# Optimization experiments

Measured on AMD Instinct MI355X. Metric: run time of the kernel, lower is better.

## Reference

```python
import jax, jax.numpy as jnp
import numpy as np

N_TREE = 200
DEPTH = 3
N_LEAF = 2 ** (DEPTH + 1) - 1      # 15 internal decision nodes
N_LEAVES = N_LEAF + 1              # 16 leaves
N_NODE = 64
BATCH = 2048
D_FEAT = 512
LR = 0.01


def _leaf_paths(depth):
    """For each of the 2^(depth+1) leaves, the internal-node index and the
    left/right bit at every level (matches the tf.gather index construction:
    bit==0 -> take p, bit==1 -> take 1-p; children of node n are 2n+1, 2n+2)."""
    L = 2 ** (depth + 1)
    nodes = np.zeros((L, depth + 1), np.int32)
    bits = np.zeros((L, depth + 1), np.int32)
    for l in range(L):
        node = 0
        for d in range(depth + 1):
            bit = (l >> (depth - d)) & 1
            nodes[l, d] = node
            bits[l, d] = bit
            node = 2 * node + 1 + bit
    return nodes, bits

_NODES, _BITS = _leaf_paths(DEPTH)


def setup_inputs() -> dict:
    key = jax.random.key(0)
    ks = jax.random.split(key, 9)
    u = lambda k, s: jax.random.uniform(k, s, jnp.float32, -0.05, 0.05)  # keras 'uniform' init
    return {
        "x": jax.random.normal(ks[0], (BATCH, D_FEAT), jnp.float32),
        "y_true": jax.random.normal(ks[1], (BATCH, 1), jnp.float32),
        "w_t": u(ks[2], (N_TREE, D_FEAT, N_NODE)),
        "b_t": u(ks[3], (N_TREE, N_NODE)),
        "w_d": u(ks[4], (N_TREE, N_NODE, N_LEAF)),
        "b_d": u(ks[5], (N_TREE, N_LEAF)),
        "w_l": u(ks[6], (N_TREE, N_LEAVES)),
        "b_l": u(ks[7], (N_TREE,)),
        "f_0": jnp.full((1,), 0.5, jnp.float32),
    }


def reference(x, y_true, w_t, b_t, w_d, b_d, w_l, b_l, f_0):
    B = x.shape[0]
    # Batched per-tree small MLP (the 200-iteration Python loop in the original).
    # Dropout is identity at inference.
    h = jax.nn.relu(jnp.einsum('bd,tdn->tbn', x, w_t) + b_t[:, None, :])        # [T,B,N_NODE]
    p = jax.nn.sigmoid(jnp.einsum('tbn,tnl->tbl', h, w_d) + b_d[:, None, :])    # [T,B,15]
    # Soft binary-tree routing: mu[t,b,leaf] = prod over path of p or (1-p).
    # This reproduces the tiled-index tf.gather construction exactly.
    pn = p[..., _NODES]                                                         # [T,B,16,DEPTH+1]
    q = jnp.where(_BITS == 1, 1.0 - pn, pn)
    mu = jnp.prod(q, axis=-1)                                                   # [T,B,16]
    # Per-tree leaf score with tanh.
    f = jnp.tanh(jnp.einsum('tbl,tl->tb', mu, w_l) + b_l[:, None])              # [T,B]
    # Sequential boosting accumulation: predict_k = f_0 + lr * sum_{i<k} f_i.
    cum = f_0 + LR * jnp.cumsum(f.T, axis=1)                                    # [B,T]
    py_x = jnp.concatenate([jnp.broadcast_to(f_0[None, :], (B, 1)), cum], axis=1)  # [B,T+1]
    return py_x
```

## Files before the change

kernel.cpp:

```cpp
#include <hip/hip_runtime.h>

#define T_TREES 200
#define BATCH   2048
#define D_FEAT  512
#define N_NODE  64
#define LR      0.01f

typedef __attribute__((__ext_vector_type__(8)))  __bf16 bf16x8;
typedef __attribute__((__ext_vector_type__(16))) float  f32x16;

__device__ __forceinline__ unsigned short f32_to_bf16(float f) {
    unsigned u = __float_as_uint(f);
    u += 0x7FFFu + ((u >> 16) & 1u);
    return (unsigned short)(u >> 16);
}

__device__ __forceinline__ void gload_lds16(const void* g, void* l) {
    __builtin_amdgcn_global_load_lds(
        (__attribute__((address_space(1))) void*)(void*)g,
        (__attribute__((address_space(3))) void*)l,
        16, 0, 0);
}


__global__ __launch_bounds__(256) void prep_x(const float* __restrict__ x,
                                              unsigned short* __restrict__ x_p) {
    __shared__ float tile[64 * 65];
    int mb = blockIdx.x >> 3;
    int slab = blockIdx.x & 7;
    const float* src = x + (mb * 64) * D_FEAT + slab * 64;
    #pragma unroll
    for (int p = 0; p < 16; ++p) {
        int idx = p * 256 + threadIdx.x;
        int r = idx >> 6, c = idx & 63;
        tile[r * 65 + c] = src[r * D_FEAT + c];
    }
    __syncthreads();
    int mt = mb >> 1, mq = mb & 1;
    unsigned short* dst = x_p + mt * 65536 + slab * 8192 + mq * 512;
    #pragma unroll
    for (int p = 0; p < 8; ++p) {
        int idx = p * 256 + threadIdx.x;
        int kgl = idx >> 8;
        int r   = (idx >> 2) & 63;
        int jp  = idx & 3;
        ushort2 o;
        o.x = f32_to_bf16(tile[r * 65 + kgl * 8 + jp * 2]);
        o.y = f32_to_bf16(tile[r * 65 + kgl * 8 + jp * 2 + 1]);
        *(ushort2*)(dst + kgl * 1024 + r * 8 + jp * 2) = o;
    }
}

__global__ __launch_bounds__(256) void prep_wt(const float* __restrict__ w_t,
                                               unsigned short* __restrict__ w_p) {
    __shared__ float tile[64 * 65];
    int t = blockIdx.x >> 3, slab = blockIdx.x & 7;
    const float* src = w_t + t * (D_FEAT * N_NODE) + slab * 64 * N_NODE;
    #pragma unroll
    for (int p = 0; p < 16; ++p) {
        int idx = p * 256 + threadIdx.x;
        int d = idx >> 6, n = idx & 63;
        tile[d * 65 + n] = src[d * N_NODE + n];
    }
    __syncthreads();
    unsigned short* dst = w_p + (t >> 1) * 65536 + slab * 8192 + (t & 1) * 512;
    #pragma unroll
    for (int p = 0; p < 8; ++p) {
        int idx = p * 256 + threadIdx.x;
        int kgl = idx >> 8;
        int n   = (idx >> 2) & 63;
        int jp  = idx & 3;
        ushort2 o;
        o.x = f32_to_bf16(tile[(kgl * 8 + jp * 2) * 65 + n]);
        o.y = f32_to_bf16(tile[(kgl * 8 + jp * 2 + 1) * 65 + n]);
        *(ushort2*)(dst + kgl * 1024 + n * 8 + jp * 2) = o;
    }
}

__global__ void prep_wd(const float* __restrict__ w_d, unsigned short* __restrict__ w_dt) {
    int i = blockIdx.x * 256 + threadIdx.x;
    int n = i & 63;
    int l = (i >> 6) & 31;
    int t = i >> 11;
    float v = (l < 15) ? w_d[(t * 64 + n) * 15 + l] : 0.f;
    w_dt[i] = f32_to_bf16(v);
}

__global__ __launch_bounds__(256, 3) void gbdt_main(
    const unsigned short* __restrict__ x_p,
    const unsigned short* __restrict__ w_p,
    const unsigned short* __restrict__ w_dt,
    const float* __restrict__ b_t,
    const float* __restrict__ b_d,
    const float* __restrict__ w_l,
    const float* __restrict__ b_l,
    float* __restrict__ f_ws)
{
    __shared__ alignas(16) char smem[36864];
    unsigned short* Hs = (unsigned short*)smem;
    float*          Pf = (float*)smem;

    const int tid    = threadIdx.x;
    const int lane   = tid & 63;
    const int w      = tid >> 6;
    const int lane31 = lane & 31;
    const int kh     = lane >> 5;
    const int wm     = w >> 1;
    const int wn     = w & 1;

    const int xcd  = blockIdx.x & 7;
    const int slot = blockIdx.x >> 3;
    const int mt   = slot & 15;
    const int pj   = slot >> 4;
    const int pair = xcd * 13 + pj;
    if (pair >= 100) return;
    const int t0 = pair * 2;
    const int m0 = mt * 128;

    const char* ga = (const char*)(x_p + mt * 65536) + tid * 16;
    const char* gb = (const char*)(w_p + pair * 65536) + tid * 16;

    f32x16 acc[2][2];
    #pragma unroll
    for (int mb = 0; mb < 2; ++mb)
        #pragma unroll
        for (int nb = 0; nb < 2; ++nb)
            acc[mb][nb] = (f32x16)(0.f);

    #pragma unroll
    for (int i = 0; i < 2; ++i) {
        gload_lds16(ga + i * 4096, smem + tid * 16 + i * 4096);
        gload_lds16(gb + i * 4096, smem + 8192 + tid * 16 + i * 4096);
    }

    const int aoff = (wm * 64 + lane31) * 16;
    const int boff = 8192 + (wn * 64 + lane31) * 16;

    for (int c = 0; c < 16; ++c) {
        __syncthreads();
        if (c < 15) {
            char* nx = smem + ((c + 1) & 1) * 16384;
            #pragma unroll
            for (int i = 0; i < 2; ++i) {
                gload_lds16(ga + (c + 1) * 8192 + i * 4096, nx + tid * 16 + i * 4096);
                gload_lds16(gb + (c + 1) * 8192 + i * 4096, nx + 8192 + tid * 16 + i * 4096);
            }
        }
        const char* buf = smem + (c & 1) * 16384;
        #pragma unroll
        for (int s2 = 0; s2 < 2; ++s2) {
            const int kgl = 2 * s2 + kh;
            bf16x8 av[2], bv[2];
            #pragma unroll
            for (int mb = 0; mb < 2; ++mb)
                av[mb] = *(const bf16x8*)(buf + aoff + kgl * 2048 + mb * 512);
            #pragma unroll
            for (int nb = 0; nb < 2; ++nb)
                bv[nb] = *(const bf16x8*)(buf + boff + kgl * 2048 + nb * 512);
            #pragma unroll
            for (int mb = 0; mb < 2; ++mb)
                #pragma unroll
                for (int nb = 0; nb < 2; ++nb)
                    acc[mb][nb] = __builtin_amdgcn_mfma_f32_32x32x16_bf16(
                        av[mb], bv[nb], acc[mb][nb], 0, 0, 0);
        }
    }

    __syncthreads();

    #pragma unroll
    for (int nb = 0; nb < 2; ++nb) {
        float btv = b_t[(t0 + wn) * 64 + nb * 32 + lane31];
        #pragma unroll
        for (int mb = 0; mb < 2; ++mb)
            #pragma unroll
            for (int r = 0; r < 16; ++r) {
                int m = wm * 64 + mb * 32 + (r & 3) + 8 * (r >> 2) + 4 * kh;
                float h = fmaxf(acc[mb][nb][r] + btv, 0.f);
                Hs[wn * 8704 + m * 68 + nb * 32 + lane31] = f32_to_bf16(h);
            }
    }
    __syncthreads();

    f32x16 acc2[2] = { (f32x16)(0.f), (f32x16)(0.f) };
    const unsigned short* pW = w_dt + (t0 + wn) * 2048 + lane31 * 64 + kh * 8;
    #pragma unroll
    for (int s = 0; s < 4; ++s) {
        bf16x8 bv = *(const bf16x8*)(pW + s * 16);
        #pragma unroll
        for (int i = 0; i < 2; ++i) {
            const unsigned short* pH =
                Hs + wn * 8704 + (wm * 64 + i * 32 + lane31) * 68 + s * 16 + kh * 8;
            bf16x8 av = *(const bf16x8*)pH;
            acc2[i] = __builtin_amdgcn_mfma_f32_32x32x16_bf16(av, bv, acc2[i], 0, 0, 0);
        }
    }
    __syncthreads();

    if (lane31 < 15) {
        float bdv = b_d[(t0 + wn) * 15 + lane31];
        #pragma unroll
        for (int i = 0; i < 2; ++i)
            #pragma unroll
            for (int r = 0; r < 16; ++r) {
                int m = wm * 64 + i * 32 + (r & 3) + 8 * (r >> 2) + 4 * kh;
                float lg = acc2[i][r] + bdv;
                Pf[(wn * 128 + m) * 17 + lane31] = 1.f / (1.f + __expf(-lg));
            }
    }
    __syncthreads();

    {
        int m = tid & 127;
        int j = tid >> 7;
        int t = t0 + j;
        float pv[15];
        #pragma unroll
        for (int i = 0; i < 15; ++i) pv[i] = Pf[(j * 128 + m) * 17 + i];
        float facc = 0.f;
        #pragma unroll
        for (int leaf = 0; leaf < 16; ++leaf) {
            float mu = 1.f;
            int node = 0;
            #pragma unroll
            for (int d = 0; d < 4; ++d) {
                int bit = (leaf >> (3 - d)) & 1;
                float p = pv[node];
                mu *= bit ? (1.f - p) : p;
                node = 2 * node + 1 + bit;
            }
            facc += mu * w_l[t * 16 + leaf];
        }
        f_ws[(m0 + m) * T_TREES + t] = tanhf(facc + b_l[t]);
    }
}

__global__ void scan_k(const float* __restrict__ f_ws, const float* __restrict__ f0p,
                       float* __restrict__ out) {
    int b = blockIdx.x, tid = threadIdx.x;
    int lane = tid & 63, wid = tid >> 6;
    float f0 = f0p[0];
    float x = (tid < T_TREES) ? f_ws[b * T_TREES + tid] : 0.f;
    #pragma unroll
    for (int off = 1; off < 64; off <<= 1) {
        float y = __shfl_up(x, off, 64);
        if (lane >= off) x += y;
    }
    __shared__ float wsum[4];
    if (lane == 63) wsum[wid] = x;
    __syncthreads();
    float base = 0.f;
    for (int i = 0; i < wid; ++i) base += wsum[i];
    float incl = x + base;
    if (tid == 0) out[b * (T_TREES + 1)] = f0;
    if (tid < T_TREES) out[b * (T_TREES + 1) + 1 + tid] = f0 + LR * incl;
}

extern "C" void kernel_launch(void* const* d_in, const int* in_sizes, int n_in,
                              void* d_out, int out_size, void* d_ws, size_t ws_size,
                              hipStream_t stream) {
    const float* x   = (const float*)d_in[0];
    const float* w_t = (const float*)d_in[2];
    const float* b_t = (const float*)d_in[3];
    const float* w_d = (const float*)d_in[4];
    const float* b_d = (const float*)d_in[5];
    const float* w_l = (const float*)d_in[6];
    const float* b_l = (const float*)d_in[7];
    const float* f_0 = (const float*)d_in[8];
    float* out = (float*)d_out;

    char* ws = (char*)d_ws;
    unsigned short* x_p  = (unsigned short*)(ws);
    unsigned short* w_p  = (unsigned short*)(ws + 2097152);
    unsigned short* w_dt = (unsigned short*)(ws + 15204352);
    float*          f_ws = (float*)(ws + 16023552);

    prep_x  <<< 256, 256, 0, stream>>>(x, x_p);
    prep_wt <<<1600, 256, 0, stream>>>(w_t, w_p);
    prep_wd <<<1600, 256, 0, stream>>>(w_d, w_dt);
    gbdt_main<<<1664, 256, 0, stream>>>(x_p, w_p, w_dt, b_t, b_d, w_l, b_l, f_ws);
    scan_k<<<BATCH, 256, 0, stream>>>(f_ws, f_0, out);
}
```

Baseline: 134.1 us.

## Merge prep kernels and load A operand directly into registers

Fuses the three preprocessing kernels into a single launch with block-range dispatch, removing two kernel launches. In the main GEMM, the x tile is now read straight from global memory into registers and double-buffered there, while only the weight tile goes through LDS. This halves the LDS staging buffer, which lowers shared memory use and lets the launch bound ask for 4 blocks per CU instead of 3. The trade-off is more register pressure and direct global loads of A that are not coalesced through LDS.

```diff
diff --git a/kernel.cpp b/kernel.cpp
--- a/kernel.cpp
+++ b/kernel.cpp
@@ -22,71 +22,70 @@
         16, 0, 0);
 }
 
-
-__global__ __launch_bounds__(256) void prep_x(const float* __restrict__ x,
-                                              unsigned short* __restrict__ x_p) {
+__global__ __launch_bounds__(256) void prep_all(
+    const float* __restrict__ x, const float* __restrict__ w_t,
+    const float* __restrict__ w_d,
+    unsigned short* __restrict__ x_p, unsigned short* __restrict__ w_p,
+    unsigned short* __restrict__ w_dt) {
     __shared__ float tile[64 * 65];
-    int mb = blockIdx.x >> 3;
-    int slab = blockIdx.x & 7;
-    const float* src = x + (mb * 64) * D_FEAT + slab * 64;
-    #pragma unroll
-    for (int p = 0; p < 16; ++p) {
-        int idx = p * 256 + threadIdx.x;
-        int r = idx >> 6, c = idx & 63;
-        tile[r * 65 + c] = src[r * D_FEAT + c];
-    }
-    __syncthreads();
-    int mt = mb >> 1, mq = mb & 1;
-    unsigned short* dst = x_p + mt * 65536 + slab * 8192 + mq * 512;
-    #pragma unroll
-    for (int p = 0; p < 8; ++p) {
-        int idx = p * 256 + threadIdx.x;
-        int kgl = idx >> 8;
-        int r   = (idx >> 2) & 63;
-        int jp  = idx & 3;
-        ushort2 o;
-        o.x = f32_to_bf16(tile[r * 65 + kgl * 8 + jp * 2]);
-        o.y = f32_to_bf16(tile[r * 65 + kgl * 8 + jp * 2 + 1]);
-        *(ushort2*)(dst + kgl * 1024 + r * 8 + jp * 2) = o;
-    }
-}
-
-__global__ __launch_bounds__(256) void prep_wt(const float* __restrict__ w_t,
-                                               unsigned short* __restrict__ w_p) {
-    __shared__ float tile[64 * 65];
-    int t = blockIdx.x >> 3, slab = blockIdx.x & 7;
-    const float* src = w_t + t * (D_FEAT * N_NODE) + slab * 64 * N_NODE;
-    #pragma unroll
-    for (int p = 0; p < 16; ++p) {
-        int idx = p * 256 + threadIdx.x;
-        int d = idx >> 6, n = idx & 63;
-        tile[d * 65 + n] = src[d * N_NODE + n];
-    }
-    __syncthreads();
-    unsigned short* dst = w_p + (t >> 1) * 65536 + slab * 8192 + (t & 1) * 512;
-    #pragma unroll
-    for (int p = 0; p < 8; ++p) {
-        int idx = p * 256 + threadIdx.x;
-        int kgl = idx >> 8;
-        int n   = (idx >> 2) & 63;
-        int jp  = idx & 3;
-        ushort2 o;
-        o.x = f32_to_bf16(tile[(kgl * 8 + jp * 2) * 65 + n]);
-        o.y = f32_to_bf16(tile[(kgl * 8 + jp * 2 + 1) * 65 + n]);
-        *(ushort2*)(dst + kgl * 1024 + n * 8 + jp * 2) = o;
-    }
-}
-
-__global__ void prep_wd(const float* __restrict__ w_d, unsigned short* __restrict__ w_dt) {
-    int i = blockIdx.x * 256 + threadIdx.x;
-    int n = i & 63;
-    int l = (i >> 6) & 31;
-    int t = i >> 11;
-    float v = (l < 15) ? w_d[(t * 64 + n) * 15 + l] : 0.f;
-    w_dt[i] = f32_to_bf16(v);
-}
-
-__global__ __launch_bounds__(256, 3) void gbdt_main(
+    int b = blockIdx.x;
+    if (b < 256) {
+        int mb = b >> 3, slab = b & 7;
+        const float* src = x + (mb * 64) * D_FEAT + slab * 64;
+        #pragma unroll
+        for (int p = 0; p < 16; ++p) {
+            int idx = p * 256 + threadIdx.x;
+            int r = idx >> 6, c = idx & 63;
+            tile[r * 65 + c] = src[r * D_FEAT + c];
+        }
+        __syncthreads();
+        int mt = mb >> 1, mq = mb & 1;
+        unsigned short* dst = x_p + mt * 65536 + slab * 8192 + mq * 512;
+        #pragma unroll
+        for (int p = 0; p < 8; ++p) {
+            int idx = p * 256 + threadIdx.x;
+            int kgl = idx >> 8;
+            int r   = (idx >> 2) & 63;
+            int jp  = idx & 3;
+            ushort2 o;
+            o.x = f32_to_bf16(tile[r * 65 + kgl * 8 + jp * 2]);
+            o.y = f32_to_bf16(tile[r * 65 + kgl * 8 + jp * 2 + 1]);
+            *(ushort2*)(dst + kgl * 1024 + r * 8 + jp * 2) = o;
+        }
+    } else if (b < 1856) {
+        int bb = b - 256;
+        int t = bb >> 3, slab = bb & 7;
+        const float* src = w_t + t * (D_FEAT * N_NODE) + slab * 64 * N_NODE;
+        #pragma unroll
+        for (int p = 0; p < 16; ++p) {
+            int idx = p * 256 + threadIdx.x;
+            int d = idx >> 6, n = idx & 63;
+            tile[d * 65 + n] = src[d * N_NODE + n];
+        }
+        __syncthreads();
+        unsigned short* dst = w_p + (t >> 1) * 65536 + slab * 8192 + (t & 1) * 512;
+        #pragma unroll
+        for (int p = 0; p < 8; ++p) {
+            int idx = p * 256 + threadIdx.x;
+            int kgl = idx >> 8;
+            int n   = (idx >> 2) & 63;
+            int jp  = idx & 3;
+            ushort2 o;
+            o.x = f32_to_bf16(tile[(kgl * 8 + jp * 2) * 65 + n]);
+            o.y = f32_to_bf16(tile[(kgl * 8 + jp * 2 + 1) * 65 + n]);
+            *(ushort2*)(dst + kgl * 1024 + n * 8 + jp * 2) = o;
+        }
+    } else {
+        int i = (b - 1856) * 256 + threadIdx.x;
+        int n = i & 63;
+        int l = (i >> 6) & 31;
+        int t = i >> 11;
+        float v = (l < 15) ? w_d[(t * 64 + n) * 15 + l] : 0.f;
+        w_dt[i] = f32_to_bf16(v);
+    }
+}
+
+__global__ __launch_bounds__(256, 4) void gbdt_main(
     const unsigned short* __restrict__ x_p,
     const unsigned short* __restrict__ w_p,
     const unsigned short* __restrict__ w_dt,
@@ -96,7 +95,7 @@
     const float* __restrict__ b_l,
     float* __restrict__ f_ws)
 {
-    __shared__ alignas(16) char smem[36864];
+    __shared__ alignas(16) char smem[34816];
     unsigned short* Hs = (unsigned short*)smem;
     float*          Pf = (float*)smem;
 
@@ -117,7 +116,7 @@
     const int t0 = pair * 2;
     const int m0 = mt * 128;
 
-    const char* ga = (const char*)(x_p + mt * 65536) + tid * 16;
+    const unsigned short* pA = x_p + mt * 65536 + kh * 1024 + (wm * 64 + lane31) * 8;
     const char* gb = (const char*)(w_p + pair * 65536) + tid * 16;
 
     f32x16 acc[2][2];
@@ -127,43 +126,45 @@
         for (int nb = 0; nb < 2; ++nb)
             acc[mb][nb] = (f32x16)(0.f);
 
-    #pragma unroll
-    for (int i = 0; i < 2; ++i) {
-        gload_lds16(ga + i * 4096, smem + tid * 16 + i * 4096);
-        gload_lds16(gb + i * 4096, smem + 8192 + tid * 16 + i * 4096);
-    }
-
-    const int aoff = (wm * 64 + lane31) * 16;
-    const int boff = 8192 + (wn * 64 + lane31) * 16;
+    bf16x8 a_cur[4], a_nxt[4];
+    #pragma unroll
+    for (int s2 = 0; s2 < 2; ++s2)
+        #pragma unroll
+        for (int mb = 0; mb < 2; ++mb)
+            a_cur[s2 * 2 + mb] = *(const bf16x8*)(pA + s2 * 2048 + mb * 256);
+    gload_lds16(gb, smem + tid * 16);
+    gload_lds16(gb + 4096, smem + tid * 16 + 4096);
 
     for (int c = 0; c < 16; ++c) {
         __syncthreads();
         if (c < 15) {
-            char* nx = smem + ((c + 1) & 1) * 16384;
-            #pragma unroll
-            for (int i = 0; i < 2; ++i) {
-                gload_lds16(ga + (c + 1) * 8192 + i * 4096, nx + tid * 16 + i * 4096);
-                gload_lds16(gb + (c + 1) * 8192 + i * 4096, nx + 8192 + tid * 16 + i * 4096);
-            }
-        }
-        const char* buf = smem + (c & 1) * 16384;
+            char* nx = smem + ((c + 1) & 1) * 8192;
+            gload_lds16(gb + (c + 1) * 8192, nx + tid * 16);
+            gload_lds16(gb + (c + 1) * 8192 + 4096, nx + tid * 16 + 4096);
+            #pragma unroll
+            for (int s2 = 0; s2 < 2; ++s2)
+                #pragma unroll
+                for (int mb = 0; mb < 2; ++mb)
+                    a_nxt[s2 * 2 + mb] =
+                        *(const bf16x8*)(pA + (c + 1) * 4096 + s2 * 2048 + mb * 256);
+        }
+        const char* buf = smem + (c & 1) * 8192;
         #pragma unroll
         for (int s2 = 0; s2 < 2; ++s2) {
             const int kgl = 2 * s2 + kh;
-            bf16x8 av[2], bv[2];
-            #pragma unroll
-            for (int mb = 0; mb < 2; ++mb)
-                av[mb] = *(const bf16x8*)(buf + aoff + kgl * 2048 + mb * 512);
+            bf16x8 bv[2];
             #pragma unroll
             for (int nb = 0; nb < 2; ++nb)
-                bv[nb] = *(const bf16x8*)(buf + boff + kgl * 2048 + nb * 512);
+                bv[nb] = *(const bf16x8*)(buf + (kgl * 128 + wn * 64 + nb * 32 + lane31) * 16);
             #pragma unroll
             for (int mb = 0; mb < 2; ++mb)
                 #pragma unroll
                 for (int nb = 0; nb < 2; ++nb)
                     acc[mb][nb] = __builtin_amdgcn_mfma_f32_32x32x16_bf16(
-                        av[mb], bv[nb], acc[mb][nb], 0, 0, 0);
-        }
+                        a_cur[s2 * 2 + mb], bv[nb], acc[mb][nb], 0, 0, 0);
+        }
+        #pragma unroll
+        for (int i = 0; i < 4; ++i) a_cur[i] = a_nxt[i];
     }
 
     __syncthreads();
@@ -275,9 +276,7 @@
     unsigned short* w_dt = (unsigned short*)(ws + 15204352);
     float*          f_ws = (float*)(ws + 16023552);
 
-    prep_x  <<< 256, 256, 0, stream>>>(x, x_p);
-    prep_wt <<<1600, 256, 0, stream>>>(w_t, w_p);
-    prep_wd <<<1600, 256, 0, stream>>>(w_d, w_dt);
+    prep_all<<<3456, 256, 0, stream>>>(x, w_t, w_d, x_p, w_p, w_dt);
     gbdt_main<<<1664, 256, 0, stream>>>(x_p, w_p, w_dt, b_t, b_d, w_l, b_l, f_ws);
     scan_k<<<BATCH, 256, 0, stream>>>(f_ws, f_0, out);
 }
```

Measured after the change: 131.1 us. -2.3%, faster.
